# Kernel tuning notes

Measured on AMD Instinct MI355X. Metric: run time of the kernel, lower is better.

Reference implementation:

```python
import jax, jax.numpy as jnp
import numpy as np

N = 50000      # nodes
E = 150000     # edges
D = 64         # d_model
ED = 16        # edge_attr dim
EPS = 1e-5


def setup_inputs() -> dict:
    key = jax.random.key(0)
    ks = jax.random.split(key, 12)
    s = lambda k, shape, fan: jax.random.normal(k, shape, jnp.float32) * (1.0 / np.sqrt(fan))
    return {
        "x": jax.random.normal(ks[0], (N, D), jnp.float32),
        "edge_index": jax.random.randint(ks[1], (2, E), 0, N),
        "edge_attr": jax.random.normal(ks[2], (E, ED), jnp.float32),
        # edge MLP: Linear(ED, D*D)
        "W_edge": s(ks[3], (ED, D * D), ED),
        "b_edge": jnp.zeros((D * D,), jnp.float32),
        # NNConv root linear (bias=False in PyG) + conv bias
        "W_root": s(ks[4], (D, D), D),
        "bias": jnp.zeros((D,), jnp.float32),
        # residual linear
        "W_res": s(ks[5], (D, D), D),
        "b_res": jnp.zeros((D,), jnp.float32),
        # LayerNorm
        "gamma": jnp.ones((D,), jnp.float32),
        "beta": jnp.zeros((D,), jnp.float32),
    }


def reference(x, edge_index, edge_attr, W_edge, b_edge, W_root, bias, W_res, b_res, gamma, beta):
    src, dst = edge_index[0], edge_index[1]
    # residual branch (dropout is identity in eval mode)
    x_res = x @ W_res + b_res                                  # [N, D]
    # per-edge dynamic weight matrices from edge MLP
    We = (edge_attr @ W_edge + b_edge).reshape(E, D, D)        # [E, D, D]
    # gather source feats, per-edge matmul, scatter-add to dst
    msg = jnp.einsum('ed,edf->ef', x[src], We)                 # [E, D]
    agg = jax.ops.segment_sum(msg, dst, num_segments=N)        # [N, D]
    conv = agg + x @ W_root + bias                             # NNConv root + bias
    # fused residual + LayerNorm
    h = conv + x_res
    mu = jnp.mean(h, axis=-1, keepdims=True)
    var = jnp.mean((h - mu) ** 2, axis=-1, keepdims=True)
    return (h - mu) * jax.lax.rsqrt(var + EPS) * gamma + beta
```

## Files before the change

### kernel.cpp

```cpp
#include <hip/hip_runtime.h>
#include <stdint.h>


typedef _Float16 half8 __attribute__((ext_vector_type(8)));
typedef float floatx4 __attribute__((ext_vector_type(4)));

union HFrag { half8 h8; uint32_t u[4]; uint4 u4; };

__device__ __forceinline__ uint32_t pk_f16(float lo, float hi) {
  auto h = __builtin_amdgcn_cvt_pkrtz(lo, hi);
  union { decltype(h) h2; uint32_t u; } cv;
  cv.h2 = h;
  return cv.u;
}

__device__ __forceinline__ uint32_t pk_mul_f16(uint32_t a, uint32_t b) {
  uint32_t r;
  asm("v_pk_mul_f16 %0, %1, %2" : "=v"(r) : "v"(a), "v"(b));
  return r;
}

__device__ __forceinline__ uint32_t cvt_pk_bf16(float lo, float hi) {
  uint32_t r;
  asm("v_cvt_pk_bf16_f32 %0, %1, %2" : "=v"(r) : "v"(lo), "v"(hi));
  return r;
}

__device__ __forceinline__ uint16_t f32_to_bf16_bits(float x) {
  uint32_t u = __float_as_uint(x);
  u += 0x7fffu + ((u >> 16) & 1u);
  return (uint16_t)(u >> 16);
}

#define W2FRAG_OFF 0
#define XBF_OFF    148480
#define PREP_ELEMS 69632
#define PREP_BLOCKS 272

__global__ __launch_bounds__(256) void k1_kernel(
    const float* __restrict__ x,
    const float* __restrict__ W_edge, const float* __restrict__ b_edge,
    const float* __restrict__ W_root, const float* __restrict__ bias,
    const float* __restrict__ W_res,  const float* __restrict__ b_res,
    uint16_t* __restrict__ w2frag, float* __restrict__ out,
    uint32_t* __restrict__ xpk, int N) {
  int tid = threadIdx.x;
  if (blockIdx.x < PREP_BLOCKS) {
    int gid = blockIdx.x * 256 + tid;
    if (gid < PREP_ELEMS) {
      int i = gid & 7, l = (gid >> 3) & 63, c = (gid >> 9) & 3;
      int t = (gid >> 11) & 1, s = gid >> 12;
      int d = t * 32 + 8 * (l >> 4) + i;
      int f = c * 16 + (l & 15);
      float v = (s < 16) ? W_edge[s * 4096 + d * 64 + f] : b_edge[d * 64 + f];
      w2frag[gid] = (uint16_t)(pk_f16(v, 0.f) & 0xffffu);
    }
    return;
  }
  typedef short short8 __attribute__((ext_vector_type(8)));
  union AFrag { short8 s8; uint32_t u[4]; };
  int bb = blockIdx.x - PREP_BLOCKS;
  int w = tid >> 6, l = tid & 63;
  int l16 = l & 15, lq = l >> 4;
  union BF { short8 s8; uint16_t h[8]; } Bf[2][4];
#pragma unroll
  for (int t = 0; t < 2; ++t)
#pragma unroll
    for (int c = 0; c < 4; ++c)
#pragma unroll
      for (int i = 0; i < 8; ++i) {
        int d = t * 32 + 8 * lq + i;
        int f = c * 16 + l16;
        Bf[t][c].h[i] = f32_to_bf16_bits(W_root[d * 64 + f] + W_res[d * 64 + f]);
      }
  int arow = bb * 64 + w * 16 + l16;
  float xv[16];
#pragma unroll
  for (int t = 0; t < 2; ++t)
#pragma unroll
    for (int i = 0; i < 8; ++i)
      xv[t * 8 + i] = (arow < N) ? x[arow * 64 + t * 32 + 8 * lq + i] : 0.0f;
  if (xpk != nullptr && arow < N) {
#pragma unroll
    for (int t = 0; t < 2; ++t) {
      uint4 c;
      c.x = pk_f16(xv[t * 8 + 0], xv[t * 8 + 1]);
      c.y = pk_f16(xv[t * 8 + 2], xv[t * 8 + 3]);
      c.z = pk_f16(xv[t * 8 + 4], xv[t * 8 + 5]);
      c.w = pk_f16(xv[t * 8 + 6], xv[t * 8 + 7]);
      *(uint4*)(xpk + arow * 32 + t * 16 + lq * 4) = c;
    }
  }
  AFrag A[2];
#pragma unroll
  for (int t = 0; t < 2; ++t)
#pragma unroll
    for (int j = 0; j < 4; ++j)
      A[t].u[j] = cvt_pk_bf16(xv[t * 8 + 2 * j], xv[t * 8 + 2 * j + 1]);
  floatx4 acc[4];
#pragma unroll
  for (int c = 0; c < 4; ++c) acc[c] = (floatx4){0.f, 0.f, 0.f, 0.f};
#pragma unroll
  for (int t = 0; t < 2; ++t)
#pragma unroll
    for (int c = 0; c < 4; ++c)
      acc[c] = __builtin_amdgcn_mfma_f32_16x16x32_bf16(A[t].s8, Bf[t][c].s8, acc[c], 0, 0, 0);
#pragma unroll
  for (int c = 0; c < 4; ++c) {
    int f = c * 16 + l16;
    float bs = bias[f] + b_res[f];
#pragma unroll
    for (int r = 0; r < 4; ++r) {
      int row = bb * 64 + w * 16 + lq * 4 + r;
      if (row < N) out[row * 64 + f] = acc[c][r] + bs;
    }
  }
}

template <int XPK>
__global__ __launch_bounds__(256, 2) void edge_kernel(
    const float* __restrict__ x, const uint32_t* __restrict__ xpk,
    const int* __restrict__ eidx, const float* __restrict__ attr,
    const uint16_t* __restrict__ w2frag, float* __restrict__ out, int E) {
  __shared__ uint32_t xp_lds[64][36];
  __shared__ uint32_t a_pk[64][20];
  __shared__ int      dst_lds[64];
  __shared__ float    red[4][32][68];

  int tid = threadIdx.x;
  int w = tid >> 6, l = tid & 63, l16 = l & 15, lq = l >> 4;
  int row = tid >> 2, q = tid & 3;
  const int* srcp = eidx;
  const int* dstp = eidx + E;
  const float4* x4 = (const float4*)x;
  const float4* a4 = (const float4*)attr;
  int T = (E + 63) >> 6;
  const half8* bp = (const half8*)w2frag;

  half8 Breg[4][2][4];
#pragma unroll
  for (int si = 0; si < 4; ++si) {
    int s = 4 * si + w;
#pragma unroll
    for (int t = 0; t < 2; ++t)
#pragma unroll
      for (int c = 0; c < 4; ++c)
        Breg[si][t][c] = bp[((s * 2 + t) * 4 + c) * 64 + l];
  }
  int tx = w - 2;
  half8 Bx[4];
  if (tx >= 0) {
#pragma unroll
    for (int c = 0; c < 4; ++c) Bx[c] = bp[((32 + tx) * 4 + c) * 64 + l];
  }

  int tl = blockIdx.x;
  if (tl < T) {
    int cnt0 = min(64, E - tl * 64);
    bool ok = row < cnt0;
    int sidx = ok ? srcp[tl * 64 + row] : 0;
    uint4 u0 = make_uint4(0, 0, 0, 0), u1 = make_uint4(0, 0, 0, 0);
    if (XPK) {
      if (ok) {
        u0 = *(const uint4*)(xpk + sidx * 32 + q * 8);
        u1 = *(const uint4*)(xpk + sidx * 32 + q * 8 + 4);
      }
    } else if (ok) {
      float4 v0 = x4[sidx * 16 + q * 4 + 0], v1 = x4[sidx * 16 + q * 4 + 1];
      float4 v2 = x4[sidx * 16 + q * 4 + 2], v3 = x4[sidx * 16 + q * 4 + 3];
      u0 = make_uint4(pk_f16(v0.x, v0.y), pk_f16(v0.z, v0.w),
                      pk_f16(v1.x, v1.y), pk_f16(v1.z, v1.w));
      u1 = make_uint4(pk_f16(v2.x, v2.y), pk_f16(v2.z, v2.w),
                      pk_f16(v3.x, v3.y), pk_f16(v3.z, v3.w));
    }
    *(uint4*)&xp_lds[row][q * 8] = u0;
    *(uint4*)&xp_lds[row][q * 8 + 4] = u1;
    float4 av = make_float4(0.f, 0.f, 0.f, 0.f);
    if (ok) av = a4[(tl * 64 + row) * 4 + q];
    a_pk[row][q * 4 + 0] = pk_f16(av.x, av.x);
    a_pk[row][q * 4 + 1] = pk_f16(av.y, av.y);
    a_pk[row][q * 4 + 2] = pk_f16(av.z, av.z);
    a_pk[row][q * 4 + 3] = pk_f16(av.w, av.w);
    if (tid < 64) dst_lds[tid] = (tid < cnt0) ? dstp[tl * 64 + tid] : 0;
  }
  __syncthreads();

  for (; tl < T; tl += gridDim.x) {
    int cnt = min(64, E - tl * 64);
    int nxt = tl + (int)gridDim.x;
    bool havenxt = nxt < T;
    float4 xr[4];
    uint4 xu0 = make_uint4(0, 0, 0, 0), xu1 = make_uint4(0, 0, 0, 0);
    float4 ar = make_float4(0.f, 0.f, 0.f, 0.f);
    int dv = 0;
    if (havenxt) {
      int cntn = min(64, E - nxt * 64);
      bool ok = row < cntn;
      int sidx = ok ? srcp[nxt * 64 + row] : 0;
      if (XPK) {
        if (ok) {
          xu0 = *(const uint4*)(xpk + sidx * 32 + q * 8);
          xu1 = *(const uint4*)(xpk + sidx * 32 + q * 8 + 4);
        }
      } else {
#pragma unroll
        for (int j = 0; j < 4; ++j) {
          xr[j] = make_float4(0.f, 0.f, 0.f, 0.f);
          if (ok) xr[j] = x4[sidx * 16 + q * 4 + j];
        }
      }
      if (ok) ar = a4[(nxt * 64 + row) * 4 + q];
      if (ok) dv = dstp[nxt * 64 + row];
    }

#pragma unroll
    for (int p = 0; p < 2; ++p) {
      floatx4 acc[2][4];
#pragma unroll
      for (int rt = 0; rt < 2; ++rt)
#pragma unroll
        for (int c = 0; c < 4; ++c) acc[rt][c] = (floatx4){0.f, 0.f, 0.f, 0.f};

#pragma unroll
      for (int rt = 0; rt < 2; ++rt) {
        int arow = p * 32 + rt * 16 + l16;
        uint4 xp0 = *(const uint4*)&xp_lds[arow][lq * 4];
        uint4 xp1 = *(const uint4*)&xp_lds[arow][16 + lq * 4];
#pragma unroll
        for (int si = 0; si < 4; ++si) {
          uint32_t apk = a_pk[arow][4 * si + w];
          HFrag A0, A1;
          A0.u[0] = pk_mul_f16(xp0.x, apk);
          A0.u[1] = pk_mul_f16(xp0.y, apk);
          A0.u[2] = pk_mul_f16(xp0.z, apk);
          A0.u[3] = pk_mul_f16(xp0.w, apk);
          A1.u[0] = pk_mul_f16(xp1.x, apk);
          A1.u[1] = pk_mul_f16(xp1.y, apk);
          A1.u[2] = pk_mul_f16(xp1.z, apk);
          A1.u[3] = pk_mul_f16(xp1.w, apk);
#pragma unroll
          for (int c = 0; c < 4; ++c) {
            acc[rt][c] = __builtin_amdgcn_mfma_f32_16x16x32_f16(
                A0.h8, Breg[si][0][c], acc[rt][c], 0, 0, 0);
            acc[rt][c] = __builtin_amdgcn_mfma_f32_16x16x32_f16(
                A1.h8, Breg[si][1][c], acc[rt][c], 0, 0, 0);
          }
        }
        if (tx >= 0) {
          HFrag Ax;
          Ax.u4 = (tx == 0) ? xp0 : xp1;
#pragma unroll
          for (int c = 0; c < 4; ++c)
            acc[rt][c] = __builtin_amdgcn_mfma_f32_16x16x32_f16(
                Ax.h8, Bx[c], acc[rt][c], 0, 0, 0);
        }
      }

#pragma unroll
      for (int rt = 0; rt < 2; ++rt)
#pragma unroll
        for (int c = 0; c < 4; ++c) {
          int f = c * 16 + l16;
#pragma unroll
          for (int r = 0; r < 4; ++r)
            red[w][rt * 16 + lq * 4 + r][f] = acc[rt][c][r];
        }
      __syncthreads();

#pragma unroll
      for (int c = 0; c < 4; ++c) {
        int f = c * 16 + l16;
#pragma unroll
        for (int r = 0; r < 2; ++r) {
          int rr = w * 8 + lq * 2 + r;
          float s = red[0][rr][f] + red[1][rr][f] + red[2][rr][f] + red[3][rr][f];
          int grow = p * 32 + rr;
          if (grow < cnt) atomicAdd(&out[dst_lds[grow] * 64 + f], s);
        }
      }
      __syncthreads();
    }

    if (havenxt) {
      if (XPK) {
        *(uint4*)&xp_lds[row][q * 8] = xu0;
        *(uint4*)&xp_lds[row][q * 8 + 4] = xu1;
      } else {
        uint4 u0 = make_uint4(pk_f16(xr[0].x, xr[0].y), pk_f16(xr[0].z, xr[0].w),
                              pk_f16(xr[1].x, xr[1].y), pk_f16(xr[1].z, xr[1].w));
        uint4 u1 = make_uint4(pk_f16(xr[2].x, xr[2].y), pk_f16(xr[2].z, xr[2].w),
                              pk_f16(xr[3].x, xr[3].y), pk_f16(xr[3].z, xr[3].w));
        *(uint4*)&xp_lds[row][q * 8] = u0;
        *(uint4*)&xp_lds[row][q * 8 + 4] = u1;
      }
      a_pk[row][q * 4 + 0] = pk_f16(ar.x, ar.x);
      a_pk[row][q * 4 + 1] = pk_f16(ar.y, ar.y);
      a_pk[row][q * 4 + 2] = pk_f16(ar.z, ar.z);
      a_pk[row][q * 4 + 3] = pk_f16(ar.w, ar.w);
      if (q == 0) dst_lds[row] = dv;
    }
    __syncthreads();
  }
}

__global__ __launch_bounds__(256) void ln_kernel(
    float* __restrict__ out, const float* __restrict__ gamma,
    const float* __restrict__ beta, int N) {
  int w = threadIdx.x >> 6, l = threadIdx.x & 63;
  int row = blockIdx.x * 4 + w;
  if (row >= N) return;
  float v = out[row * 64 + l];
  float s = v;
#pragma unroll
  for (int m = 32; m >= 1; m >>= 1) s += __shfl_xor(s, m);
  float mu = s * 0.015625f;
  float d = v - mu;
  float q = d * d;
#pragma unroll
  for (int m = 32; m >= 1; m >>= 1) q += __shfl_xor(q, m);
  float var = q * 0.015625f;
  out[row * 64 + l] = d * rsqrtf(var + 1e-5f) * gamma[l] + beta[l];
}

extern "C" void kernel_launch(void* const* d_in, const int* in_sizes, int n_in,
                              void* d_out, int out_size, void* d_ws, size_t ws_size,
                              hipStream_t stream) {
  const float* x      = (const float*)d_in[0];
  const int*   eidx   = (const int*)d_in[1];
  const float* attr   = (const float*)d_in[2];
  const float* W_edge = (const float*)d_in[3];
  const float* b_edge = (const float*)d_in[4];
  const float* W_root = (const float*)d_in[5];
  const float* bias   = (const float*)d_in[6];
  const float* W_res  = (const float*)d_in[7];
  const float* b_res  = (const float*)d_in[8];
  const float* gamma  = (const float*)d_in[9];
  const float* beta   = (const float*)d_in[10];
  int N = in_sizes[0] / 64;
  int E = in_sizes[1] / 2;
  float* out = (float*)d_out;
  uint16_t* w2frag = (uint16_t*)((char*)d_ws + W2FRAG_OFF);

  size_t need = (size_t)XBF_OFF + (size_t)N * 128;
  bool usepk = ws_size >= need;
  uint32_t* xpk = usepk ? (uint32_t*)((char*)d_ws + XBF_OFF) : nullptr;

  int nBase = (N + 63) / 64;
  k1_kernel<<<PREP_BLOCKS + nBase, 256, 0, stream>>>(
      x, W_edge, b_edge, W_root, bias, W_res, b_res, w2frag, out, xpk, N);
  int T = (E + 63) / 64;
  int G = T < 512 ? T : 512;
  if (usepk)
    edge_kernel<1><<<G, 256, 0, stream>>>(x, xpk, eidx, attr, w2frag, out, E);
  else
    edge_kernel<0><<<G, 256, 0, stream>>>(x, xpk, eidx, attr, w2frag, out, E);
  ln_kernel<<<(N + 3) / 4, 256, 0, stream>>>(out, gamma, beta, N);
}
```

Before: 73.24 us.

## Fuse LayerNorm into edge kernel via cooperative grid sync

Merges the separate LayerNorm kernel into the edge scatter kernel. The edge kernel becomes a cooperative launch, and a grid-wide sync runs before a grid-strided LayerNorm pass over the output rows. This drops one kernel launch and its scheduling gap. In exchange it adds the cost of a grid barrier, and the LayerNorm pass now runs on at most 512 blocks instead of N/4 blocks. The host also queries occupancy on every call.

```diff
diff --git a/kernel.cpp b/kernel.cpp
--- a/kernel.cpp
+++ b/kernel.cpp
@@ -1,6 +1,9 @@
 #include <hip/hip_runtime.h>
+#include <hip/hip_cooperative_groups.h>
 #include <stdint.h>
 
+
+namespace cg = cooperative_groups;
 
 typedef _Float16 half8 __attribute__((ext_vector_type(8)));
 typedef float floatx4 __attribute__((ext_vector_type(4)));
@@ -118,10 +121,11 @@
 }
 
 template <int XPK>
-__global__ __launch_bounds__(256, 2) void edge_kernel(
+__global__ __launch_bounds__(256, 2) void edge_ln_kernel(
     const float* __restrict__ x, const uint32_t* __restrict__ xpk,
     const int* __restrict__ eidx, const float* __restrict__ attr,
-    const uint16_t* __restrict__ w2frag, float* __restrict__ out, int E) {
+    const uint16_t* __restrict__ w2frag, float* __restrict__ out, int E,
+    const float* __restrict__ gamma, const float* __restrict__ beta, int N) {
   __shared__ uint32_t xp_lds[64][36];
   __shared__ uint32_t a_pk[64][20];
   __shared__ int      dst_lds[64];
@@ -301,25 +305,23 @@
     }
     __syncthreads();
   }
-}
-
-__global__ __launch_bounds__(256) void ln_kernel(
-    float* __restrict__ out, const float* __restrict__ gamma,
-    const float* __restrict__ beta, int N) {
-  int w = threadIdx.x >> 6, l = threadIdx.x & 63;
-  int row = blockIdx.x * 4 + w;
-  if (row >= N) return;
-  float v = out[row * 64 + l];
-  float s = v;
-#pragma unroll
-  for (int m = 32; m >= 1; m >>= 1) s += __shfl_xor(s, m);
-  float mu = s * 0.015625f;
-  float d = v - mu;
-  float q = d * d;
-#pragma unroll
-  for (int m = 32; m >= 1; m >>= 1) q += __shfl_xor(q, m);
-  float var = q * 0.015625f;
-  out[row * 64 + l] = d * rsqrtf(var + 1e-5f) * gamma[l] + beta[l];
+
+  cg::this_grid().sync();
+
+  float gm = gamma[l], bt = beta[l];
+  for (int r = blockIdx.x * 4 + w; r < N; r += gridDim.x * 4) {
+    float v = out[r * 64 + l];
+    float s = v;
+#pragma unroll
+    for (int m = 32; m >= 1; m >>= 1) s += __shfl_xor(s, m);
+    float mu = s * 0.015625f;
+    float d = v - mu;
+    float qv = d * d;
+#pragma unroll
+    for (int m = 32; m >= 1; m >>= 1) qv += __shfl_xor(qv, m);
+    float var = qv * 0.015625f;
+    out[r * 64 + l] = d * rsqrtf(var + 1e-5f) * gm + bt;
+  }
 }
 
 extern "C" void kernel_launch(void* const* d_in, const int* in_sizes, int n_in,
@@ -348,11 +350,25 @@
   int nBase = (N + 63) / 64;
   k1_kernel<<<PREP_BLOCKS + nBase, 256, 0, stream>>>(
       x, W_edge, b_edge, W_root, bias, W_res, b_res, w2frag, out, xpk, N);
+
   int T = (E + 63) / 64;
-  int G = T < 512 ? T : 512;
+  int maxB = 0;
   if (usepk)
-    edge_kernel<1><<<G, 256, 0, stream>>>(x, xpk, eidx, attr, w2frag, out, E);
+    (void)hipOccupancyMaxActiveBlocksPerMultiprocessor(&maxB, edge_ln_kernel<1>, 256, 0);
   else
-    edge_kernel<0><<<G, 256, 0, stream>>>(x, xpk, eidx, attr, w2frag, out, E);
-  ln_kernel<<<(N + 3) / 4, 256, 0, stream>>>(out, gamma, beta, N);
-}
+    (void)hipOccupancyMaxActiveBlocksPerMultiprocessor(&maxB, edge_ln_kernel<0>, 256, 0);
+  if (maxB < 1) maxB = 1;
+  int G = maxB * 256;
+  if (G > 512) G = 512;
+  if (G > T) G = T;
+
+  void* kargs[] = {(void*)&x, (void*)&xpk, (void*)&eidx, (void*)&attr,
+                   (void*)&w2frag, (void*)&out, (void*)&E,
+                   (void*)&gamma, (void*)&beta, (void*)&N};
+  if (usepk)
+    (void)hipLaunchCooperativeKernel((void*)edge_ln_kernel<1>, dim3(G), dim3(256),
+                                     kargs, 0, stream);
+  else
+    (void)hipLaunchCooperativeKernel((void*)edge_ln_kernel<0>, dim3(G), dim3(256),
+                                     kargs, 0, stream);
+}
```

Measured after the change: 132.1 us. 1.8x slower.
